# Optimization experiments

Measured on AMD Instinct MI355X. Metric: run time of the kernel, lower is better.

Reference implementation:

```python
import jax, jax.numpy as jnp
import numpy as np

# symmetry-function hyperparameters (match module defaults), meshgrid order as in TF code
_LAMBD_INIT = np.array([1.0, -1.0])
_ITA_INIT = np.array([4.0])
_ZETA_INIT = np.array([2.0, 4.0, 8.0])
_lg, _ig, _zg = np.meshgrid(_LAMBD_INIT, _ITA_INIT, _ZETA_INIT)
LAMBD = jnp.asarray(_lg.flatten(), dtype=jnp.float32)  # [L], L = 6
ITA = jnp.asarray(_ig.flatten(), dtype=jnp.float32)
ZETA = jnp.asarray(_zg.flatten(), dtype=jnp.float32)

B, M = 16, 64  # batch, max_atoms


def setup_inputs() -> dict:
    key = jax.random.key(0)
    k1, k2, k3 = jax.random.split(key, 3)
    d_cutoff = jax.random.uniform(k1, (B, M, M), dtype=jnp.float32)
    d = jax.random.uniform(k2, (B, M, M), dtype=jnp.float32)
    atom_coordinates = jax.random.normal(k3, (B, M, 3), dtype=jnp.float32)
    return {"d_cutoff": d_cutoff, "d": d, "atom_coordinates": atom_coordinates}


def reference(d_cutoff, d, atom_coordinates):
    # pairwise displacement vectors: [B, M, M, 3]
    vec = atom_coordinates[:, :, None, :] - atom_coordinates[:, None, :, :]
    # broadcastable triple-distance views [B, M(i), M(j), M(k)]
    R_ij = d[:, :, :, None]
    R_ik = d[:, :, None, :]
    R_jk = d[:, None, :, :]
    # theta = (r_ij . r_ik) / (R_ij * R_ik + eps)   (cosine ratio; original then takes cos of it)
    theta = jnp.einsum('bijd,bikd->bijk', vec, vec) / (R_ij * R_ik + 1e-5)
    sum_sq = R_ij * R_ij + R_ik * R_ik + R_jk * R_jk  # [B, M, M, M]
    f_prod = (d_cutoff[:, :, :, None] * d_cutoff[:, :, None, :]
              * d_cutoff[:, None, :, :])  # [B, M, M, M]
    lambd = LAMBD.reshape(1, 1, 1, 1, -1)
    ita = ITA.reshape(1, 1, 1, 1, -1)
    zeta = ZETA.reshape(1, 1, 1, 1, -1)
    # faithful to original: cos is applied to the cosine ratio itself
    out = (jnp.power(1.0 + lambd * jnp.cos(theta)[..., None], zeta)
           * jnp.exp(-ita * sum_sq[..., None])
           * f_prod[..., None])  # [B, M, M, M, L]
    res = out.sum(axis=(2, 3)) * jnp.power(jnp.float32(2.0), 1.0 - ZETA.reshape(1, 1, -1))
    return res  # [B, M, L]
```

## Files before the change

kernel.cpp:

```cpp
#include <hip/hip_runtime.h>
#include <hip/hip_bf16.h>
#include <math.h>


#define BB 16
#define MM 64
#define PP 6

__device__ __forceinline__ float fast_cos(float x) {
    double xd = (double)x;
    double fn = rint(xd * 0.63661977236758138243);
    float  r  = (float)fma(-fn, 1.5707963267948966, xd);
    int    q  = ((int)fn) & 3;
    float  z  = r * r;
    float s = r + r * z * (-1.6666666641626524e-01f + z * (8.3333293858894632e-03f
              + z * (-1.9839334836096632e-04f + z * 2.7183114939898219e-06f)));
    float c = 1.0f + z * (-4.9999999725103100e-01f + z * (4.1666623323739063e-02f
              + z * (-1.3886763774609929e-03f + z * 2.4390448796277409e-05f)));
    float mag = (q & 1) ? s : c;
    return __int_as_float(__float_as_int(mag) ^ (((q + 1) & 2) << 30));
}

__global__ __launch_bounds__(256) void angsym_kernel(
    const float* __restrict__ d_cutoff,
    const float* __restrict__ d,
    const float* __restrict__ coords,
    float* __restrict__ out)
{
    __shared__ float4 Vrow[MM];
    __shared__ float  Arow[MM];
    __shared__ float  Tmat[MM * MM];
    __shared__ float  red[4 * PP];

    const int blk = blockIdx.x;
    const int b = blk >> 6;
    const int i = blk & 63;
    const int t = threadIdx.x;

    const float* __restrict__ db = d        + b * MM * MM;
    const float* __restrict__ cb = d_cutoff + b * MM * MM;

    if (t < MM) {
        const float* cc = coords + b * MM * 3;
        float dv = db[i * MM + t];
        Arow[t] = expf(-4.0f * dv * dv) * cb[i * MM + t];
        Vrow[t] = make_float4(cc[i * 3 + 0] - cc[t * 3 + 0],
                              cc[i * 3 + 1] - cc[t * 3 + 1],
                              cc[i * 3 + 2] - cc[t * 3 + 2],
                              dv);
    }
    __syncthreads();

    #pragma unroll
    for (int s = 0; s < (MM * MM) / 256; ++s) {
        int idx = t + s * 256;
        int j = idx >> 6, k = idx & 63;
        float dv = db[idx];
        float g  = expf(-4.0f * dv * dv) * cb[idx];
        Tmat[idx] = g * Arow[j] * Arow[k];
    }
    __syncthreads();

    const int k  = t & 63;
    const int jb = t >> 6;
    const float4 Vk = Vrow[k];

    float a0 = 0.f, a1 = 0.f, a2 = 0.f, a3 = 0.f, a4 = 0.f, a5 = 0.f;

    #pragma unroll
    for (int s = 0; s < 16; ++s) {
        const int j = jb + (s << 2);
        float4 Vj = Vrow[j];
        float dot = Vj.x * Vk.x + Vj.y * Vk.y + Vj.z * Vk.z;
        float den = Vj.w * Vk.w + 1e-5f;
        float th  = dot / den;
        float c   = fast_cos(th);
        float w   = Tmat[j * MM + k];
        float u = 1.0f + c, v = 1.0f - c;
        float u2 = u * u,  v2 = v * v;
        float u4 = u2 * u2, v4 = v2 * v2;
        float u8 = u4 * u4, v8 = v4 * v4;
        a0 += u2 * w; a1 += u4 * w; a2 += u8 * w;
        a3 += v2 * w; a4 += v4 * w; a5 += v8 * w;
    }

    #pragma unroll
    for (int off = 32; off > 0; off >>= 1) {
        a0 += __shfl_down(a0, off);
        a1 += __shfl_down(a1, off);
        a2 += __shfl_down(a2, off);
        a3 += __shfl_down(a3, off);
        a4 += __shfl_down(a4, off);
        a5 += __shfl_down(a5, off);
    }

    const int wave = t >> 6;
    const int lane = t & 63;
    if (lane == 0) {
        red[wave * PP + 0] = a0;
        red[wave * PP + 1] = a1;
        red[wave * PP + 2] = a2;
        red[wave * PP + 3] = a3;
        red[wave * PP + 4] = a4;
        red[wave * PP + 5] = a5;
    }
    __syncthreads();

    if (t < PP) {
        float s = red[t] + red[PP + t] + red[2 * PP + t] + red[3 * PP + t];
        const float scale = (t % 3 == 0) ? 0.5f : ((t % 3 == 1) ? 0.125f : 0.0078125f);
        out[(b * MM + i) * PP + t] = s * scale;
    }
}

extern "C" void kernel_launch(void* const* d_in, const int* in_sizes, int n_in,
                              void* d_out, int out_size, void* d_ws, size_t ws_size,
                              hipStream_t stream) {
    const float* d_cutoff = (const float*)d_in[0];
    const float* d        = (const float*)d_in[1];
    const float* coords   = (const float*)d_in[2];
    float* out            = (float*)d_out;

    angsym_kernel<<<BB * MM, 256, 0, stream>>>(d_cutoff, d, coords, out);
}
```

Before: 64.71 us.

## Exploit j/k symmetry to halve cosine and power evaluations per block

The integrand's angle term is symmetric in j and k, so the kernel now visits each unordered (j,k) pair once and weights it by the sum of both Tmat entries. Pairs are enumerated with a round-robin tournament scheme over 63 rows plus a fixed element, and the diagonal is handled in a separate pass by the first 64 threads. This roughly halves the fast_cos and power work. In exchange it adds index arithmetic, a second LDS read, and idle threads in the last iteration and in the diagonal pass.

Result: no change. 63.88 us (-1.3%).

```diff
diff --git a/kernel.cpp b/kernel.cpp
--- a/kernel.cpp
+++ b/kernel.cpp
@@ -19,6 +19,16 @@
               + z * (-1.3886763774609929e-03f + z * 2.4390448796277409e-05f)));
     float mag = (q & 1) ? s : c;
     return __int_as_float(__float_as_int(mag) ^ (((q + 1) & 2) << 30));
+}
+
+__device__ __forceinline__ void accum_powers(float c, float w,
+    float& a0, float& a1, float& a2, float& a3, float& a4, float& a5) {
+    float u = 1.0f + c, v = 1.0f - c;
+    float u2 = u * u,  v2 = v * v;
+    float u4 = u2 * u2, v4 = v2 * v2;
+    float u8 = u4 * u4, v8 = v4 * v4;
+    a0 += u2 * w; a1 += u4 * w; a2 += u8 * w;
+    a3 += v2 * w; a4 += v4 * w; a5 += v8 * w;
 }
 
 __global__ __launch_bounds__(256) void angsym_kernel(
@@ -61,27 +71,37 @@
     }
     __syncthreads();
 
-    const int k  = t & 63;
-    const int jb = t >> 6;
-    const float4 Vk = Vrow[k];
+    const int hl = t & 31;
+    const int g  = t >> 5;
 
     float a0 = 0.f, a1 = 0.f, a2 = 0.f, a3 = 0.f, a4 = 0.f, a5 = 0.f;
 
     #pragma unroll
-    for (int s = 0; s < 16; ++s) {
-        const int j = jb + (s << 2);
-        float4 Vj = Vrow[j];
+    for (int s = 0; s < 8; ++s) {
+        const int r = g + (s << 3);
+        if (r >= 63) continue;
+        int p1, p2;
+        if (hl == 0) { p1 = 63; p2 = r; }
+        else {
+            p1 = r + hl; if (p1 >= 63) p1 -= 63;
+            p2 = r - hl; if (p2 < 0)   p2 += 63;
+        }
+        float4 Vj = Vrow[p1];
+        float4 Vk = Vrow[p2];
         float dot = Vj.x * Vk.x + Vj.y * Vk.y + Vj.z * Vk.z;
         float den = Vj.w * Vk.w + 1e-5f;
-        float th  = dot / den;
-        float c   = fast_cos(th);
-        float w   = Tmat[j * MM + k];
-        float u = 1.0f + c, v = 1.0f - c;
-        float u2 = u * u,  v2 = v * v;
-        float u4 = u2 * u2, v4 = v2 * v2;
-        float u8 = u4 * u4, v8 = v4 * v4;
-        a0 += u2 * w; a1 += u4 * w; a2 += u8 * w;
-        a3 += v2 * w; a4 += v4 * w; a5 += v8 * w;
+        float c   = fast_cos(dot / den);
+        float w   = Tmat[p1 * MM + p2] + Tmat[p2 * MM + p1];
+        accum_powers(c, w, a0, a1, a2, a3, a4, a5);
+    }
+
+    if (t < MM) {
+        float4 Vd = Vrow[t];
+        float dot = Vd.x * Vd.x + Vd.y * Vd.y + Vd.z * Vd.z;
+        float den = Vd.w * Vd.w + 1e-5f;
+        float c   = fast_cos(dot / den);
+        float w   = Tmat[t * MM + t];
+        accum_powers(c, w, a0, a1, a2, a3, a4, a5);
     }
 
     #pragma unroll
```
